# Optimization experiments

Hardware: AMD Instinct MI355X
Metric: run time of the kernel (lower is better)

The kernel has to match this reference:

```python
import jax, jax.numpy as jnp
import numpy as np

EPS = 1e-12  # torch F.normalize eps

def _l2norm(t):
    # normalize over last axis (tokens N), matching F.normalize(dim=-1)
    n = jnp.sqrt(jnp.sum(t * t, axis=-1, keepdims=True))
    return t / jnp.maximum(n, EPS)

def setup_inputs() -> dict:
    key = jax.random.key(0)
    ks = jax.random.split(key, 4)
    B, N, C, H = 16, 3136, 768, 16
    x = jax.random.normal(ks[0], (B, N, C), dtype=jnp.float32)
    w_qkv = jax.random.normal(ks[1], (3 * C, C), dtype=jnp.float32) * (C ** -0.5)
    temperature = jnp.ones((H, 1, 1), dtype=jnp.float32)
    w_proj = jax.random.normal(ks[2], (C, C), dtype=jnp.float32) * (C ** -0.5)
    b_proj = jnp.zeros((C,), dtype=jnp.float32)
    return {"x": x, "w_qkv": w_qkv, "temperature": temperature,
            "w_proj": w_proj, "b_proj": b_proj}

def reference(x, w_qkv, temperature, w_proj, b_proj):
    B, N, C = x.shape
    H = temperature.shape[0]
    dh = C // H
    # qkv: [B,N,3C] -> [B,N,3,H,dh] -> [3,B,H,dh,N]
    qkv = (x @ w_qkv.T).reshape(B, N, 3, H, dh)
    qkv = jnp.transpose(qkv, (2, 0, 3, 4, 1))
    q, k, v = qkv[0], qkv[1], qkv[2]          # each [B,H,dh,N]
    q = _l2norm(q)
    k = _l2norm(k)
    # cross-covariance attention over channel axis: [B,H,dh,dh]
    attn = jnp.einsum('bhdn,bhen->bhde', q, k) * temperature
    attn = jax.nn.softmax(attn, axis=-1)
    out = jnp.einsum('bhde,bhen->bhdn', attn, v)  # [B,H,dh,N]
    out = jnp.transpose(out, (0, 3, 1, 2)).reshape(B, N, C)
    return out @ w_proj.T + b_proj
```

## Files before the change

kernel.cpp:

```cpp
#include <hip/hip_runtime.h>
#include <hip/hip_bf16.h>
#include <stdint.h>

using f32x4   = __attribute__((ext_vector_type(4))) float;
using half8   = __attribute__((ext_vector_type(8))) _Float16;
using half4   = __attribute__((ext_vector_type(4))) _Float16;
using float4v = __attribute__((ext_vector_type(4))) float;

typedef const __attribute__((address_space(1))) void gas_void;
typedef __attribute__((address_space(3))) void las_void;

__device__ __forceinline__ void gload_lds16(const void* gptr, void* lptr) {
  __builtin_amdgcn_global_load_lds((gas_void*)(uintptr_t)gptr,
                                   (las_void*)(uintptr_t)lptr, 16, 0, 0);
}

#define MFMA_F16(a, b, c) __builtin_amdgcn_mfma_f32_16x16x32_f16((a), (b), (c), 0, 0, 0)

__global__ __launch_bounds__(256)
void k_cvtx(const float* __restrict__ x, _Float16* __restrict__ x16,
            _Float16* __restrict__ xT,
            const float* __restrict__ wqkv, const float* __restrict__ wproj,
            _Float16* __restrict__ w16, _Float16* __restrict__ wp16,
            _Float16* __restrict__ wvT) {
  const int bid = blockIdx.x;
  if (bid >= 9408) {
    const long N1 = 221184L, N2 = 73728L, N3 = 98304L;
    const long total = N1 + N2 + N3;
    for (long i = (long)(bid - 9408) * blockDim.x + threadIdx.x; i < total;
         i += 512L * blockDim.x) {
      if (i < N1 + N2) {
        const float* src; _Float16* dst; long off;
        if (i < N1) { src = wqkv;  dst = w16;  off = i; }
        else        { src = wproj; dst = wp16; off = i - N1; }
        const float4v* p = (const float4v*)(src + off * 8);
        float4v a = p[0], b = p[1];
        half8 o;
        o[0] = (_Float16)a[0]; o[1] = (_Float16)a[1]; o[2] = (_Float16)a[2]; o[3] = (_Float16)a[3];
        o[4] = (_Float16)b[0]; o[5] = (_Float16)b[1]; o[6] = (_Float16)b[2]; o[7] = (_Float16)b[3];
        *(half8*)(dst + off * 8) = o;
      } else {
        const long u = i - N1 - N2;
        const int h = (int)(u / 6144);
        const int r = (int)(u % 6144);
        const int f = r >> 3, e0 = (r & 7) * 8;
        half8 o;
        if (e0 >= 48) {
#pragma unroll
          for (int j = 0; j < 8; ++j) o[j] = (_Float16)0.f;
        } else {
#pragma unroll
          for (int j = 0; j < 8; ++j)
            o[j] = (_Float16)wqkv[(long)(1536 + h * 48 + e0 + j) * 768 + f];
        }
        *(half8*)(wvT + ((long)(h * 768 + f) * 64 + e0)) = o;
      }
    }
    return;
  }
  __shared__ _Float16 lt[64 * 68];
  const int b = bid / 588;
  const int rem = bid % 588;
  const int tt = rem / 12, ct = rem % 12;
  const long t0g = (long)b * 3136 + tt * 64;
  const int c0 = ct * 64;
  const int tid = threadIdx.x;
#pragma unroll
  for (int ch = 0; ch < 4; ++ch) {
    const int idx = tid + ch * 256;
    const int tr = idx >> 4, cg = (idx & 15) * 4;
    float4v v = *(const float4v*)&x[(t0g + tr) * 768 + c0 + cg];
    half4 hv;
    hv[0] = (_Float16)v[0]; hv[1] = (_Float16)v[1];
    hv[2] = (_Float16)v[2]; hv[3] = (_Float16)v[3];
    *(half4*)&x16[(t0g + tr) * 768 + c0 + cg] = hv;
    *(half4*)&lt[tr * 68 + cg] = hv;
  }
  __syncthreads();
  const int c = tid >> 2, tch = tid & 3;
  half8 o0, o1;
#pragma unroll
  for (int j = 0; j < 8; ++j) o0[j] = lt[(tch * 16 + j) * 68 + c];
#pragma unroll
  for (int j = 0; j < 8; ++j) o1[j] = lt[(tch * 16 + 8 + j) * 68 + c];
  _Float16* dst = xT + (long)b * 2408448 + (long)(c0 + c) * 3136 + tt * 64 + tch * 16;
  *(half8*)dst = o0;
  *(half8*)(dst + 8) = o1;
}

__global__ __launch_bounds__(512)
void k_gram(const _Float16* __restrict__ xT, _Float16* __restrict__ G) {
  __shared__ _Float16 lds[2][2][128 * 64];
  const int tid = threadIdx.x;
  const int wv = tid >> 6, lane = tid & 63;
  const int g = lane >> 4, cidx = lane & 15;
  const int wr = wv >> 2, wc = wv & 3;

  const int nwg = (int)gridDim.x;
  const int q = nwg >> 3, r = nwg & 7;
  const int xcd = (int)blockIdx.x & 7, bidx = (int)blockIdx.x >> 3;
  int wg = (xcd < r ? xcd * (q + 1) : r * (q + 1) + (xcd - r) * q) + bidx;
  const int b = wg / 21;
  int p = wg % 21;
  int mt = 0;
  while (p >= 6 - mt) { p -= 6 - mt; ++mt; }
  const int nt = mt + p;

  const _Float16* Ab = xT + (long)b * 2408448 + (long)mt * 128 * 3136;
  const _Float16* Bb = xT + (long)b * 2408448 + (long)nt * 128 * 3136;

  const int srow8 = lane >> 3;
  const int sgr8  = (lane & 7) ^ srow8;

  auto stage = [&](int buf, int kt) {
#pragma unroll
    for (int l = 0; l < 2; ++l) {
      const int chunk = l * 8 + wv;
      const long grow = chunk * 8 + srow8;
      const long koff = (long)kt * 64 + sgr8 * 8;
      gload_lds16(Ab + grow * 3136 + koff, &lds[buf][0][chunk * 512]);
      gload_lds16(Bb + grow * 3136 + koff, &lds[buf][1][chunk * 512]);
    }
  };

  f32x4 acc[4][2] = {};
  stage(0, 0);
  __syncthreads();
  for (int kt = 0; kt < 49; ++kt) {
    const int cur = kt & 1;
    if (kt + 1 < 49) stage(cur ^ 1, kt + 1);
    half8 af[4][2], bf[2][2];
#pragma unroll
    for (int ks = 0; ks < 2; ++ks) {
      const int gran = (((ks << 2) + g) ^ (cidx & 7)) * 8;
#pragma unroll
      for (int m = 0; m < 4; ++m)
        af[m][ks] = *(const half8*)&lds[cur][0][(wr * 64 + m * 16 + cidx) * 64 + gran];
#pragma unroll
      for (int n = 0; n < 2; ++n)
        bf[n][ks] = *(const half8*)&lds[cur][1][(wc * 32 + n * 16 + cidx) * 64 + gran];
    }
#pragma unroll
    for (int ks = 0; ks < 2; ++ks)
#pragma unroll
      for (int m = 0; m < 4; ++m)
#pragma unroll
        for (int n = 0; n < 2; ++n)
          acc[m][n] = MFMA_F16(af[m][ks], bf[n][ks], acc[m][n]);
    __syncthreads();
  }
  _Float16* Gb = G + (long)b * 589824;
  const long m0 = (long)mt * 128, n0 = (long)nt * 128;
#pragma unroll
  for (int m = 0; m < 4; ++m)
#pragma unroll
    for (int rr = 0; rr < 4; ++rr) {
      const long row = m0 + wr * 64 + m * 16 + g * 4 + rr;
#pragma unroll
      for (int n = 0; n < 2; ++n)
        Gb[row * 768 + n0 + wc * 32 + n * 16 + cidx] = (_Float16)acc[m][n][rr];
    }
  if (mt != nt) {
#pragma unroll
    for (int m = 0; m < 4; ++m)
#pragma unroll
      for (int n = 0; n < 2; ++n) {
        half4 hv;
#pragma unroll
        for (int rr = 0; rr < 4; ++rr) hv[rr] = (_Float16)acc[m][n][rr];
        const long col  = n0 + wc * 32 + n * 16 + cidx;
        const long row0 = m0 + wr * 64 + m * 16 + g * 4;
        *(half4*)&Gb[col * 768 + row0] = hv;
      }
  }
}

template<bool OUT_F32>
__global__ __launch_bounds__(256)
void k_g128(const _Float16* __restrict__ A, const _Float16* __restrict__ B,
            void* __restrict__ Cv, const float* __restrict__ bias,
            int Mt, int Nt, long Areal, long Astr, long Bstr, long Cstr,
            long N, long K)
{
  __shared__ _Float16 lds[2][2][128 * 32];
  const int tid = threadIdx.x;
  const int wv = tid >> 6, lane = tid & 63;
  const int g = lane >> 4, cidx = lane & 15;
  const int wr = wv >> 1, wc = wv & 1;

  const int nwg = (int)gridDim.x;
  const int q = nwg >> 3, r = nwg & 7;
  const int xcd = (int)blockIdx.x & 7, bidx = (int)blockIdx.x >> 3;
  int wg = (xcd < r ? xcd * (q + 1) : r * (q + 1) + (xcd - r) * q) + bidx;
  const int tpb = Mt * Nt;
  const int b = wg / tpb;
  const int rem = wg % tpb;
  const int mt = rem % Mt, nt = rem / Mt;
  const long m0 = (long)mt * 128, n0 = (long)nt * 128;

  const _Float16* Ab = A + b * Astr + m0 * K;
  const _Float16* Bb = B + b * Bstr + n0 * K;
  const int nkt = (int)(K >> 5);

  const int srow = lane >> 2;
  const int sgr  = (lane & 3) ^ ((lane >> 3) & 3);

  auto stage = [&](int buf, int kt) {
#pragma unroll
    for (int l = 0; l < 2; ++l) {
      const int rbase = wv * 32 + l * 16;
      const long koff = (long)kt * 32 + sgr * 8;
      gload_lds16(Ab + (long)(rbase + srow) * K + koff, &lds[buf][0][rbase * 32]);
      gload_lds16(Bb + (long)(rbase + srow) * K + koff, &lds[buf][1][rbase * 32]);
    }
  };
  const int gr = (g ^ ((cidx >> 1) & 3)) * 8;

  f32x4 acc[4][4] = {};
  stage(0, 0);
  __syncthreads();
  for (int kt = 0; kt < nkt; ++kt) {
    const int cur = kt & 1;
    if (kt + 1 < nkt) stage(cur ^ 1, kt + 1);
    half8 af[4], bf[4];
#pragma unroll
    for (int m = 0; m < 4; ++m)
      af[m] = *(const half8*)&lds[cur][0][(wr * 64 + m * 16 + cidx) * 32 + gr];
#pragma unroll
    for (int n = 0; n < 4; ++n)
      bf[n] = *(const half8*)&lds[cur][1][(wc * 64 + n * 16 + cidx) * 32 + gr];
#pragma unroll
    for (int m = 0; m < 4; ++m)
#pragma unroll
      for (int n = 0; n < 4; ++n)
        acc[m][n] = MFMA_F16(af[m], bf[n], acc[m][n]);
    __syncthreads();
  }

  float bv[4] = {0.f, 0.f, 0.f, 0.f};
  if (bias) {
#pragma unroll
    for (int n = 0; n < 4; ++n) bv[n] = bias[n0 + wc * 64 + n * 16 + cidx];
  }
  if constexpr (OUT_F32) {
    float* C = (float*)Cv + b * Cstr;
#pragma unroll
    for (int m = 0; m < 4; ++m)
#pragma unroll
      for (int rr = 0; rr < 4; ++rr) {
        const long row = m0 + wr * 64 + m * 16 + g * 4 + rr;
        if (row < Areal) {
#pragma unroll
          for (int n = 0; n < 4; ++n)
            C[row * N + n0 + wc * 64 + n * 16 + cidx] = acc[m][n][rr] + bv[n];
        }
      }
  } else {
    _Float16* C = (_Float16*)Cv + b * Cstr;
#pragma unroll
    for (int m = 0; m < 4; ++m)
#pragma unroll
      for (int rr = 0; rr < 4; ++rr) {
        const long row = m0 + wr * 64 + m * 16 + g * 4 + rr;
        if (row < Areal) {
#pragma unroll
          for (int n = 0; n < 4; ++n)
            C[row * N + n0 + wc * 64 + n * 16 + cidx] = (_Float16)acc[m][n][rr];
        }
      }
  }
}

template<bool OUT_F32>
__global__ __launch_bounds__(512, 2)
void k_gemm8p(const _Float16* __restrict__ A, const _Float16* __restrict__ B,
              void* __restrict__ Cv, const float* __restrict__ bias,
              int Mt, int Nt, long Areal, long Astr, long Bstr, long Cstr,
              long N, long K)
{
  __shared__ _Float16 lds[65536];
  const int tid  = threadIdx.x;
  const int wv   = tid >> 6, lane = tid & 63;
  const int g    = lane >> 4, cidx = lane & 15;
  const int wr   = wv >> 2, wc = wv & 3;

  const int nwg = (int)gridDim.x;
  const int q = nwg >> 3, r = nwg & 7;
  const int xcd = (int)blockIdx.x & 7, bidx = (int)blockIdx.x >> 3;
  int wg = (xcd < r ? xcd * (q + 1) : r * (q + 1) + (xcd - r) * q) + bidx;

  const int tpb = Mt * Nt;
  const int b   = wg / tpb;
  const int rem = wg - b * tpb;
  const long mt = rem % Mt, nt = rem / Mt;
  const long m0 = mt * 256, n0 = nt * 256;

  const int NT = (int)(K >> 6);
  const int NI = NT >> 1;

  const _Float16* Ab = A + b * Astr + m0 * K;
  const _Float16* Bb = B + b * Bstr + n0 * K;

  const int srow = lane >> 2;
  const int sgr  = (lane & 3) ^ ((lane >> 3) & 3);

  auto stage = [&](int op, int buf, int kh, int t) {
    const _Float16* src = op ? Bb : Ab;
    const long koff = (long)t * 64 + kh * 32 + sgr * 8;
#pragma unroll
    for (int l = 0; l < 2; ++l) {
      const int chunk = l * 8 + wv;
      gload_lds16(src + (long)(chunk * 16 + srow) * K + koff,
                  &lds[buf * 32768 + op * 16384 + kh * 8192 + chunk * 512]);
    }
  };

  const int gr  = (g ^ ((cidx >> 1) & 3)) * 8;
  const int raA = (wr * 128 + cidx) * 32 + gr;
  const int raB = 16384 + (wc * 64 + cidx) * 32 + gr;

  f32x4 acc[8][4] = {};

  stage(0, 0, 0, 0); stage(1, 0, 0, 0);
  stage(0, 0, 1, 0); stage(1, 0, 1, 0);
  stage(0, 1, 0, 1); stage(1, 1, 0, 1);
  asm volatile("s_waitcnt vmcnt(4)" ::: "memory");
  __builtin_amdgcn_sched_barrier(0);
  __builtin_amdgcn_s_barrier();

  half8 afA[4], afB[4], bfA[4], bfB[4];
#pragma unroll
  for (int mm = 0; mm < 4; ++mm) afA[mm] = *(const half8*)&lds[raA + mm * 512];
#pragma unroll
  for (int nn = 0; nn < 4; ++nn) bfA[nn] = *(const half8*)&lds[raB + nn * 512];

#define XPH(CURA, CURB, MLO, NA, NBUF, NKS, NMLO, LOADB, NB, STAGE, BDRY)      \
  {                                                                            \
    STAGE;                                                                     \
    if (BDRY) {                                                                \
      asm volatile("s_waitcnt vmcnt(4)" ::: "memory");                         \
      __builtin_amdgcn_sched_barrier(0);                                       \
    }                                                                          \
    __builtin_amdgcn_s_barrier();                                              \
    _Pragma("unroll")                                                          \
    for (int mm = 0; mm < 4; ++mm)                                             \
      NA[mm] = *(const half8*)&lds[(NBUF)*32768 + (NKS)*8192 + raA + ((NMLO)+mm)*512]; \
    if (LOADB) {                                                               \
      _Pragma("unroll")                                                        \
      for (int nn = 0; nn < 4; ++nn)                                           \
        NB[nn] = *(const half8*)&lds[(NBUF)*32768 + (NKS)*8192 + raB + nn*512]; \
    }                                                                          \
    __builtin_amdgcn_sched_barrier(0);                                         \
    __builtin_amdgcn_s_setprio(1);                                             \
    _Pragma("unroll")                                                          \
    for (int mm = 0; mm < 4; ++mm)                                             \
      _Pragma("unroll")                                                        \
      for (int nn = 0; nn < 4; ++nn)                                           \
        acc[(MLO)+mm][nn] = MFMA_F16(CURA[mm], CURB[nn], acc[(MLO)+mm][nn]);   \
    __builtin_amdgcn_s_setprio(0);                                             \
    __builtin_amdgcn_s_barrier();                                              \
  }

  for (int it = 0; it < NI; ++it) {
    const int t1c = 2 * it + 1;
    int tn2 = 2 * it + 2; if (tn2 >= NT) tn2 -= NT;
    int tn3 = 2 * it + 3; if (tn3 >= NT) tn3 -= NT;
    XPH(afA, bfA, 0, afB, 0, 0, 4, 0, bfB, stage(0, 1, 1, t1c), false)
    XPH(afB, bfA, 4, afA, 0, 1, 0, 1, bfB, stage(1, 1, 1, t1c), false)
    XPH(afA, bfB, 0, afB, 0, 1, 4, 0, bfA, stage(0, 0, 0, tn2), false)
    XPH(afB, bfB, 4, afA, 1, 0, 0, 1, bfA, stage(1, 0, 0, tn2), true )
    XPH(afA, bfA, 0, afB, 1, 0, 4, 0, bfB, stage(0, 0, 1, tn2), false)
    XPH(afB, bfA, 4, afA, 1, 1, 0, 1, bfB, stage(1, 0, 1, tn2), false)
    XPH(afA, bfB, 0, afB, 1, 1, 4, 0, bfA, stage(0, 1, 0, tn3), false)
    XPH(afB, bfB, 4, afA, 0, 0, 0, 1, bfA, stage(1, 1, 0, tn3), true )
  }
#undef XPH

  float bv[4] = {0.f, 0.f, 0.f, 0.f};
  if (bias) {
#pragma unroll
    for (int n = 0; n < 4; ++n) bv[n] = bias[n0 + wc * 64 + n * 16 + cidx];
  }
  if constexpr (OUT_F32) {
    float* C = (float*)Cv + b * Cstr;
#pragma unroll
    for (int m = 0; m < 8; ++m)
#pragma unroll
      for (int rr = 0; rr < 4; ++rr) {
        const long row = m0 + wr * 128 + m * 16 + g * 4 + rr;
        if (row < Areal) {
#pragma unroll
          for (int n = 0; n < 4; ++n)
            C[row * N + (n0 + wc * 64 + n * 16 + cidx)] = acc[m][n][rr] + bv[n];
        }
      }
  } else {
    _Float16* C = (_Float16*)Cv + b * Cstr;
#pragma unroll
    for (int m = 0; m < 8; ++m)
#pragma unroll
      for (int rr = 0; rr < 4; ++rr) {
        const long row = m0 + wr * 128 + m * 16 + g * 4 + rr;
        if (row < Areal) {
#pragma unroll
          for (int n = 0; n < 4; ++n)
            C[row * N + (n0 + wc * 64 + n * 16 + cidx)] = (_Float16)acc[m][n][rr];
        }
      }
  }
}

__global__ __launch_bounds__(256)
void k_heads(const _Float16* __restrict__ QG, const _Float16* __restrict__ w16,
             const _Float16* __restrict__ wvT, const float* __restrict__ temperature,
             _Float16* __restrict__ weffT)
{
  const int b = blockIdx.x >> 4, h = blockIdx.x & 15;
  const int tid = threadIdx.x;
  const int w = tid >> 6, lane = tid & 63;
  const int g = lane >> 4, c = lane & 15;

  __shared__ float red[4][48 * 48];
  __shared__ float redss[4][2][48];
  __shared__ float inv[2][48];
  __shared__ _Float16 Pb[48 * 64];

  const _Float16* QGq = QG + (long)b * 1179648 + (long)(h * 48) * 768;
  const _Float16* QGk = QGq + 768L * 768;
  const _Float16* Wq  = w16 + (long)(h * 48) * 768;
  const _Float16* Wk  = w16 + (long)(768 + h * 48) * 768;

  f32x4 aS[3][3] = {};
  f32x4 aq[3] = {};
  f32x4 ak[3] = {};
  for (int ks = w * 6; ks < w * 6 + 6; ++ks) {
    const int k0 = ks * 32 + g * 8;
    half8 t1[3], t3[3], wqf[3], wkf[3];
#pragma unroll
    for (int m = 0; m < 3; ++m) {
      const long ro = (long)(m * 16 + c) * 768 + k0;
      t1[m]  = *(const half8*)(QGq + ro);
      t3[m]  = *(const half8*)(QGk + ro);
      wqf[m] = *(const half8*)(Wq + ro);
      wkf[m] = *(const half8*)(Wk + ro);
    }
#pragma unroll
    for (int m = 0; m < 3; ++m) {
      aq[m] = MFMA_F16(t1[m], wqf[m], aq[m]);
      ak[m] = MFMA_F16(t3[m], wkf[m], ak[m]);
#pragma unroll
      for (int n = 0; n < 3; ++n)
        aS[m][n] = MFMA_F16(t1[m], wkf[n], aS[m][n]);
    }
  }

#pragma unroll
  for (int m = 0; m < 3; ++m) {
#pragma unroll
    for (int n = 0; n < 3; ++n)
#pragma unroll
      for (int rr = 0; rr < 4; ++rr)
        red[w][(m * 16 + g * 4 + rr) * 48 + n * 16 + c] = aS[m][n][rr];
#pragma unroll
    for (int rr = 0; rr < 4; ++rr)
      if (c == g * 4 + rr) {
        redss[w][0][m * 16 + c] = aq[m][rr];
        redss[w][1][m * 16 + c] = ak[m][rr];
      }
  }
  __syncthreads();

  if (tid < 96) {
    const int is_k = tid / 48, d = tid % 48;
    const float s = redss[0][is_k][d] + redss[1][is_k][d] + redss[2][is_k][d] + redss[3][is_k][d];
    inv[is_k][d] = 1.0f / fmaxf(sqrtf(s), 1e-12f);
  }
  __syncthreads();

  if (tid < 48) {
    const int d = tid;
    const float iq = inv[0][d] * temperature[h];
    float rowv[48];
    float mx = -3.0e38f;
#pragma unroll
    for (int e = 0; e < 48; ++e) {
      const int idx = d * 48 + e;
      float t = (red[0][idx] + red[1][idx] + red[2][idx] + red[3][idx]) * iq * inv[1][e];
      rowv[e] = t;
      mx = fmaxf(mx, t);
    }
    float sum = 0.f;
#pragma unroll
    for (int e = 0; e < 48; ++e) {
      const float pv = __expf(rowv[e] - mx);
      rowv[e] = pv;
      sum += pv;
    }
    const float is = 1.0f / sum;
#pragma unroll
    for (int e = 0; e < 48; ++e)
      Pb[d * 64 + e] = (_Float16)(rowv[e] * is);
#pragma unroll
    for (int e = 48; e < 64; ++e)
      Pb[d * 64 + e] = (_Float16)0.f;
  }
  __syncthreads();

  half8 pf[3][2];
#pragma unroll
  for (int nf = 0; nf < 3; ++nf)
#pragma unroll
    for (int ks = 0; ks < 2; ++ks)
      pf[nf][ks] = *(const half8*)&Pb[(nf * 16 + c) * 64 + ks * 32 + g * 8];

  const _Float16* wvh = wvT + (long)h * 768 * 64;
  _Float16* wout = weffT + (long)b * 589824 + h * 48;

  for (int m = 0; m < 12; ++m) {
    const int f0 = w * 192 + m * 16;
    half8 va[2];
#pragma unroll
    for (int ks = 0; ks < 2; ++ks)
      va[ks] = *(const half8*)&wvh[(long)(f0 + c) * 64 + ks * 32 + g * 8];
    f32x4 a3[3] = {};
#pragma unroll
    for (int ks = 0; ks < 2; ++ks)
#pragma unroll
      for (int nf = 0; nf < 3; ++nf)
        a3[nf] = MFMA_F16(va[ks], pf[nf][ks], a3[nf]);
#pragma unroll
    for (int nf = 0; nf < 3; ++nf)
#pragma unroll
      for (int rr = 0; rr < 4; ++rr)
        wout[(long)(f0 + g * 4 + rr) * 768 + nf * 16 + c] = (_Float16)a3[nf][rr];
  }
}

extern "C" void kernel_launch(void* const* d_in, const int* in_sizes, int n_in,
                              void* d_out, int out_size, void* d_ws, size_t ws_size,
                              hipStream_t stream)
{
  (void)in_sizes; (void)n_in; (void)out_size; (void)ws_size;
  const float* x      = (const float*)d_in[0];
  const float* w_qkv  = (const float*)d_in[1];
  const float* temp   = (const float*)d_in[2];
  const float* w_proj = (const float*)d_in[3];
  const float* b_proj = (const float*)d_in[4];
  float* out = (float*)d_out;

  char* ws = (char*)d_ws;
  _Float16* x16   = (_Float16*)(ws);
  _Float16* xT    = (_Float16*)(ws + 77070336L);
  _Float16* G     = (_Float16*)(ws + 154140672L);
  _Float16* QG    = (_Float16*)(ws + 173015040L);
  _Float16* weffT = (_Float16*)(ws + 210763776L);
  _Float16* wfin  = (_Float16*)(ws + 229638144L);
  _Float16* w16   = (_Float16*)(ws + 248512512L);
  _Float16* wp16  = (_Float16*)(ws + 252051456L);
  _Float16* wvT   = (_Float16*)(ws + 253231104L);

  k_cvtx<<<9920, 256, 0, stream>>>(x, x16, xT, w_qkv, w_proj, w16, wp16, wvT);
  k_gram<<<336, 512, 0, stream>>>(xT, G);
  k_gemm8p<false><<<288, 512, 0, stream>>>(w16, G, QG, nullptr,
                                           6, 3, 1536, 0, 589824, 1179648, 768, 768);
  k_heads<<<256, 256, 0, stream>>>(QG, w16, wvT, temp, weffT);
  k_g128<false><<<576, 256, 0, stream>>>(wp16, weffT, wfin, nullptr,
                                         6, 6, 768, 0, 589824, 589824, 768, 768);
  k_gemm8p<true><<<624, 512, 0, stream>>>(x16, wfin, out, b_proj,
                                          13, 3, 3136, 3136L * 768, 589824, 3136L * 768,
                                          768, 768);
}
```

Before: 319.7 us.

## Make final projection GEMM persistent with atomic tile queue and cross-tile prefetch

Replaces the last 624-block GEMM launch with a persistent 256-block kernel. Each block pulls output tiles from a per-XCD atomic counter and starts loading the next tile's first K-slices while finishing the current one. The goal is to hide prologue/epilogue load latency between tiles and to avoid the tail of a partial second wave. In exchange it needs a counter in workspace reset by an extra memset, reuses xT's memory for that counter, and uses launch bounds of one block per CU.

```diff
diff --git a/kernel.cpp b/kernel.cpp
--- a/kernel.cpp
+++ b/kernel.cpp
@@ -271,69 +271,6 @@
   }
 }
 
-template<bool OUT_F32>
-__global__ __launch_bounds__(512, 2)
-void k_gemm8p(const _Float16* __restrict__ A, const _Float16* __restrict__ B,
-              void* __restrict__ Cv, const float* __restrict__ bias,
-              int Mt, int Nt, long Areal, long Astr, long Bstr, long Cstr,
-              long N, long K)
-{
-  __shared__ _Float16 lds[65536];
-  const int tid  = threadIdx.x;
-  const int wv   = tid >> 6, lane = tid & 63;
-  const int g    = lane >> 4, cidx = lane & 15;
-  const int wr   = wv >> 2, wc = wv & 3;
-
-  const int nwg = (int)gridDim.x;
-  const int q = nwg >> 3, r = nwg & 7;
-  const int xcd = (int)blockIdx.x & 7, bidx = (int)blockIdx.x >> 3;
-  int wg = (xcd < r ? xcd * (q + 1) : r * (q + 1) + (xcd - r) * q) + bidx;
-
-  const int tpb = Mt * Nt;
-  const int b   = wg / tpb;
-  const int rem = wg - b * tpb;
-  const long mt = rem % Mt, nt = rem / Mt;
-  const long m0 = mt * 256, n0 = nt * 256;
-
-  const int NT = (int)(K >> 6);
-  const int NI = NT >> 1;
-
-  const _Float16* Ab = A + b * Astr + m0 * K;
-  const _Float16* Bb = B + b * Bstr + n0 * K;
-
-  const int srow = lane >> 2;
-  const int sgr  = (lane & 3) ^ ((lane >> 3) & 3);
-
-  auto stage = [&](int op, int buf, int kh, int t) {
-    const _Float16* src = op ? Bb : Ab;
-    const long koff = (long)t * 64 + kh * 32 + sgr * 8;
-#pragma unroll
-    for (int l = 0; l < 2; ++l) {
-      const int chunk = l * 8 + wv;
-      gload_lds16(src + (long)(chunk * 16 + srow) * K + koff,
-                  &lds[buf * 32768 + op * 16384 + kh * 8192 + chunk * 512]);
-    }
-  };
-
-  const int gr  = (g ^ ((cidx >> 1) & 3)) * 8;
-  const int raA = (wr * 128 + cidx) * 32 + gr;
-  const int raB = 16384 + (wc * 64 + cidx) * 32 + gr;
-
-  f32x4 acc[8][4] = {};
-
-  stage(0, 0, 0, 0); stage(1, 0, 0, 0);
-  stage(0, 0, 1, 0); stage(1, 0, 1, 0);
-  stage(0, 1, 0, 1); stage(1, 1, 0, 1);
-  asm volatile("s_waitcnt vmcnt(4)" ::: "memory");
-  __builtin_amdgcn_sched_barrier(0);
-  __builtin_amdgcn_s_barrier();
-
-  half8 afA[4], afB[4], bfA[4], bfB[4];
-#pragma unroll
-  for (int mm = 0; mm < 4; ++mm) afA[mm] = *(const half8*)&lds[raA + mm * 512];
-#pragma unroll
-  for (int nn = 0; nn < 4; ++nn) bfA[nn] = *(const half8*)&lds[raB + nn * 512];
-
 #define XPH(CURA, CURB, MLO, NA, NBUF, NKS, NMLO, LOADB, NB, STAGE, BDRY)      \
   {                                                                            \
     STAGE;                                                                     \
@@ -361,6 +298,69 @@
     __builtin_amdgcn_s_barrier();                                              \
   }
 
+template<bool OUT_F32>
+__global__ __launch_bounds__(512, 2)
+void k_gemm8p(const _Float16* __restrict__ A, const _Float16* __restrict__ B,
+              void* __restrict__ Cv, const float* __restrict__ bias,
+              int Mt, int Nt, long Areal, long Astr, long Bstr, long Cstr,
+              long N, long K)
+{
+  __shared__ _Float16 lds[65536];
+  const int tid  = threadIdx.x;
+  const int wv   = tid >> 6, lane = tid & 63;
+  const int g    = lane >> 4, cidx = lane & 15;
+  const int wr   = wv >> 2, wc = wv & 3;
+
+  const int nwg = (int)gridDim.x;
+  const int q = nwg >> 3, r = nwg & 7;
+  const int xcd = (int)blockIdx.x & 7, bidx = (int)blockIdx.x >> 3;
+  int wg = (xcd < r ? xcd * (q + 1) : r * (q + 1) + (xcd - r) * q) + bidx;
+
+  const int tpb = Mt * Nt;
+  const int b   = wg / tpb;
+  const int rem = wg - b * tpb;
+  const long mt = rem % Mt, nt = rem / Mt;
+  const long m0 = mt * 256, n0 = nt * 256;
+
+  const int NT = (int)(K >> 6);
+  const int NI = NT >> 1;
+
+  const _Float16* Ab = A + b * Astr + m0 * K;
+  const _Float16* Bb = B + b * Bstr + n0 * K;
+
+  const int srow = lane >> 2;
+  const int sgr  = (lane & 3) ^ ((lane >> 3) & 3);
+
+  auto stage = [&](int op, int buf, int kh, int t) {
+    const _Float16* src = op ? Bb : Ab;
+    const long koff = (long)t * 64 + kh * 32 + sgr * 8;
+#pragma unroll
+    for (int l = 0; l < 2; ++l) {
+      const int chunk = l * 8 + wv;
+      gload_lds16(src + (long)(chunk * 16 + srow) * K + koff,
+                  &lds[buf * 32768 + op * 16384 + kh * 8192 + chunk * 512]);
+    }
+  };
+
+  const int gr  = (g ^ ((cidx >> 1) & 3)) * 8;
+  const int raA = (wr * 128 + cidx) * 32 + gr;
+  const int raB = 16384 + (wc * 64 + cidx) * 32 + gr;
+
+  f32x4 acc[8][4] = {};
+
+  stage(0, 0, 0, 0); stage(1, 0, 0, 0);
+  stage(0, 0, 1, 0); stage(1, 0, 1, 0);
+  stage(0, 1, 0, 1); stage(1, 1, 0, 1);
+  asm volatile("s_waitcnt vmcnt(4)" ::: "memory");
+  __builtin_amdgcn_sched_barrier(0);
+  __builtin_amdgcn_s_barrier();
+
+  half8 afA[4], afB[4], bfA[4], bfB[4];
+#pragma unroll
+  for (int mm = 0; mm < 4; ++mm) afA[mm] = *(const half8*)&lds[raA + mm * 512];
+#pragma unroll
+  for (int nn = 0; nn < 4; ++nn) bfA[nn] = *(const half8*)&lds[raB + nn * 512];
+
   for (int it = 0; it < NI; ++it) {
     const int t1c = 2 * it + 1;
     int tn2 = 2 * it + 2; if (tn2 >= NT) tn2 -= NT;
@@ -374,7 +374,6 @@
     XPH(afA, bfB, 0, afB, 1, 1, 4, 0, bfA, stage(0, 1, 0, tn3), false)
     XPH(afB, bfB, 4, afA, 0, 0, 0, 1, bfA, stage(1, 1, 0, tn3), true )
   }
-#undef XPH
 
   float bv[4] = {0.f, 0.f, 0.f, 0.f};
   if (bias) {
@@ -407,6 +406,117 @@
             C[row * N + (n0 + wc * 64 + n * 16 + cidx)] = (_Float16)acc[m][n][rr];
         }
       }
+  }
+}
+
+__global__ __launch_bounds__(512, 1)
+void k_final_p(const _Float16* __restrict__ A, const _Float16* __restrict__ B,
+               float* __restrict__ C, const float* __restrict__ bias,
+               int* __restrict__ ctr)
+{
+  __shared__ _Float16 lds[65536];
+  __shared__ int s_idx;
+  const int tid = threadIdx.x;
+  const int wv = tid >> 6, lane = tid & 63;
+  const int g = lane >> 4, cidx = lane & 15;
+  const int wr = wv >> 2, wc = wv & 3;
+  const int xcd = (int)blockIdx.x & 7;
+  const long K = 768;
+
+  const int srow = lane >> 2;
+  const int sgr  = (lane & 3) ^ ((lane >> 3) & 3);
+  const int gr   = (g ^ ((cidx >> 1) & 3)) * 8;
+  const int raA  = (wr * 128 + cidx) * 32 + gr;
+  const int raB  = 16384 + (wc * 64 + cidx) * 32 + gr;
+
+  const _Float16 *curA, *curB, *nxtA, *nxtB;
+  long curM0, curN0, curCo, nxtM0, nxtN0, nxtCo;
+
+  auto fetch = [&]() -> bool {
+    __syncthreads();
+    if (tid == 0) s_idx = atomicAdd(&ctr[xcd], 1);
+    __syncthreads();
+    const int idx = s_idx;
+    if (idx >= 78) return false;
+    const int wg = xcd * 78 + idx;
+    const int b = wg / 39;
+    const int rem = wg - b * 39;
+    const int mt = rem % 13, nt = rem / 13;
+    nxtM0 = (long)mt * 256; nxtN0 = (long)nt * 256;
+    nxtA  = A + (long)b * 2408448 + nxtM0 * K;
+    nxtB  = B + (long)b * 589824 + nxtN0 * K;
+    nxtCo = (long)b * 2408448;
+    return true;
+  };
+
+  auto stage = [&](int op, int buf, int kh, int t,
+                   const _Float16* As, const _Float16* Bs) {
+    const _Float16* src = op ? Bs : As;
+    const long koff = (long)t * 64 + kh * 32 + sgr * 8;
+#pragma unroll
+    for (int l = 0; l < 2; ++l) {
+      const int chunk = l * 8 + wv;
+      gload_lds16(src + (long)(chunk * 16 + srow) * K + koff,
+                  &lds[buf * 32768 + op * 16384 + kh * 8192 + chunk * 512]);
+    }
+  };
+
+  if (!fetch()) return;
+  curA = nxtA; curB = nxtB; curM0 = nxtM0; curN0 = nxtN0; curCo = nxtCo;
+  stage(0,0,0,0,curA,curB); stage(1,0,0,0,curA,curB);
+  stage(0,0,1,0,curA,curB); stage(1,0,1,0,curA,curB);
+  stage(0,1,0,1,curA,curB); stage(1,1,0,1,curA,curB);
+
+  for (;;) {
+    asm volatile("s_waitcnt vmcnt(4)" ::: "memory");
+    __builtin_amdgcn_sched_barrier(0);
+    __builtin_amdgcn_s_barrier();
+    half8 afA[4], afB[4], bfA[4], bfB[4];
+#pragma unroll
+    for (int mm = 0; mm < 4; ++mm) afA[mm] = *(const half8*)&lds[raA + mm * 512];
+#pragma unroll
+    for (int nn = 0; nn < 4; ++nn) bfA[nn] = *(const half8*)&lds[raB + nn * 512];
+    f32x4 acc[8][4] = {};
+
+    for (int it = 0; it < 5; ++it) {
+      const int t1c = 2 * it + 1, tn2 = 2 * it + 2, tn3 = 2 * it + 3;
+      XPH(afA, bfA, 0, afB, 0, 0, 4, 0, bfB, stage(0, 1, 1, t1c, curA, curB), false)
+      XPH(afB, bfA, 4, afA, 0, 1, 0, 1, bfB, stage(1, 1, 1, t1c, curA, curB), false)
+      XPH(afA, bfB, 0, afB, 0, 1, 4, 0, bfA, stage(0, 0, 0, tn2, curA, curB), false)
+      XPH(afB, bfB, 4, afA, 1, 0, 0, 1, bfA, stage(1, 0, 0, tn2, curA, curB), true )
+      XPH(afA, bfA, 0, afB, 1, 0, 4, 0, bfB, stage(0, 0, 1, tn2, curA, curB), false)
+      XPH(afB, bfA, 4, afA, 1, 1, 0, 1, bfB, stage(1, 0, 1, tn2, curA, curB), false)
+      XPH(afA, bfB, 0, afB, 1, 1, 4, 0, bfA, stage(0, 1, 0, tn3, curA, curB), false)
+      XPH(afB, bfB, 4, afA, 0, 0, 0, 1, bfA, stage(1, 1, 0, tn3, curA, curB), true )
+    }
+    const bool more = fetch();
+    if (!more) { nxtA = curA; nxtB = curB; }
+    XPH(afA, bfA, 0, afB, 0, 0, 4, 0, bfB, stage(0, 1, 1, 11, curA, curB), false)
+    XPH(afB, bfA, 4, afA, 0, 1, 0, 1, bfB, stage(1, 1, 1, 11, curA, curB), false)
+    XPH(afA, bfB, 0, afB, 0, 1, 4, 0, bfA, stage(0, 0, 0, 0,  nxtA, nxtB), false)
+    XPH(afB, bfB, 4, afA, 1, 0, 0, 1, bfA, stage(1, 0, 0, 0,  nxtA, nxtB), true )
+    XPH(afA, bfA, 0, afB, 1, 0, 4, 0, bfB, stage(0, 0, 1, 0,  nxtA, nxtB), false)
+    XPH(afB, bfA, 4, afA, 1, 1, 0, 1, bfB, stage(1, 0, 1, 0,  nxtA, nxtB), false)
+    XPH(afA, bfB, 0, afB, 1, 1, 4, 0, bfA, stage(0, 1, 0, 1,  nxtA, nxtB), false)
+    XPH(afB, bfB, 4, afA, 0, 0, 0, 1, bfA, stage(1, 1, 0, 1,  nxtA, nxtB), true )
+
+    float bv[4];
+#pragma unroll
+    for (int n = 0; n < 4; ++n) bv[n] = bias[curN0 + wc * 64 + n * 16 + cidx];
+    float* Cb = C + curCo;
+#pragma unroll
+    for (int m = 0; m < 8; ++m)
+#pragma unroll
+      for (int rr = 0; rr < 4; ++rr) {
+        const long row = curM0 + wr * 128 + m * 16 + g * 4 + rr;
+        if (row < 3136) {
+#pragma unroll
+          for (int n = 0; n < 4; ++n)
+            Cb[row * 768 + (curN0 + wc * 64 + n * 16 + cidx)] = acc[m][n][rr] + bv[n];
+        }
+      }
+    if (!more) return;
+    curA = nxtA; curB = nxtB; curM0 = nxtM0; curN0 = nxtN0; curCo = nxtCo;
   }
 }
 
@@ -558,15 +668,15 @@
   _Float16* w16   = (_Float16*)(ws + 248512512L);
   _Float16* wp16  = (_Float16*)(ws + 252051456L);
   _Float16* wvT   = (_Float16*)(ws + 253231104L);
+  int* ctr        = (int*)(ws + 77070336L);
 
   k_cvtx<<<9920, 256, 0, stream>>>(x, x16, xT, w_qkv, w_proj, w16, wp16, wvT);
   k_gram<<<336, 512, 0, stream>>>(xT, G);
+  hipMemsetAsync(ctr, 0, 32, stream);
   k_gemm8p<false><<<288, 512, 0, stream>>>(w16, G, QG, nullptr,
                                            6, 3, 1536, 0, 589824, 1179648, 768, 768);
   k_heads<<<256, 256, 0, stream>>>(QG, w16, wvT, temp, weffT);
   k_g128<false><<<576, 256, 0, stream>>>(wp16, weffT, wfin, nullptr,
                                          6, 6, 768, 0, 589824, 589824, 768, 768);
-  k_gemm8p<true><<<624, 512, 0, stream>>>(x16, wfin, out, b_proj,
-                                          13, 3, 3136, 3136L * 768, 589824, 3136L * 768,
-                                          768, 768);
-}
+  k_final_p<<<256, 512, 0, stream>>>(x16, wfin, out, b_proj, ctr);
+}
```

After: 334.3 us. 4.6% more time.
